# Optimization experiments

Measured on AMD Instinct MI355X. Metric: run time of the kernel, lower is better.

The kernel has to match this reference:

```python
import jax, jax.numpy as jnp
import numpy as np


def setup_inputs() -> dict:
    key = jax.random.key(0)
    k1, k2, k3 = jax.random.split(key, 3)
    B, T, D, H = 64, 512, 256, 512
    x = jax.random.normal(k1, (B, T, D), dtype=jnp.float32)
    W = jax.random.normal(k2, (D, 4 * H), dtype=jnp.float32) * 0.05
    U = jax.random.normal(k3, (H, 4 * H), dtype=jnp.float32) * 0.05
    b = jnp.zeros((4 * H,), dtype=jnp.float32)
    return {"x": x, "W": W, "U": U, "b": b, "batch": B}


def reference(x, W, U, b, batch):
    # Encoder(model_type='LSTM'): keras LSTMCell with recurrent_activation='tanh'
    # (so i/f/o gates use tanh, not sigmoid), activation='tanh'.
    B, T, D = x.shape
    H = U.shape[0]
    x_proj = jnp.einsum('btd,dk->btk', x, W) + b  # precompute input GEMM: [B,T,4H]

    def step(carry, xp_t):
        h, c = carry
        z = xp_t + h @ U                      # [B,4H]
        i, f, g, o = jnp.split(z, 4, axis=-1)  # keras gate order i,f,c,o
        i = jnp.tanh(i)
        f = jnp.tanh(f)
        g = jnp.tanh(g)
        o = jnp.tanh(o)
        c2 = f * c + i * g
        h2 = o * jnp.tanh(c2)
        return (h2, c2), h2

    h0 = jnp.zeros((B, H), dtype=x.dtype)
    c0 = jnp.zeros((B, H), dtype=x.dtype)
    (_, _), hs = jax.lax.scan(step, (h0, c0), x_proj.transpose(1, 0, 2))
    hs = hs.transpose(1, 0, 2)                              # [B,T,H]
    traj_h = jnp.concatenate([x, hs], axis=-1)              # [B,T,D+H]
    context_state = jnp.concatenate([x[:, -1, :], hs[:, -1, :]], axis=-1)  # [B,D+H]
    return context_state, traj_h
```

## Files before the change

### kernel.cpp

```cpp
#include <hip/hip_runtime.h>
#include <math.h>

#define BB 64
#define TT 512
#define DD 256
#define HH 512
#define GG 2048
#define KX 768
#define K4 192
#define CTXF 49152

__global__ void pack_vut(const float* __restrict__ Wm, const float* __restrict__ Um,
                         float* __restrict__ vut) {
    __shared__ float tile[32][33];
    int k0 = blockIdx.x * 32;
    int j0 = blockIdx.y * 32;
    int lx = threadIdx.x & 31;
    int ly = threadIdx.x >> 5;
    for (int r = ly; r < 32; r += 8) {
        int j = j0 + r, k = k0 + lx;
        tile[r][lx] = (j < DD) ? Wm[j * GG + k] : Um[(j - DD) * GG + k];
    }
    __syncthreads();
    for (int r = ly; r < 32; r += 8) {
        int k = k0 + r, j = j0 + lx;
        vut[(long)k * KX + j] = tile[lx][r];
    }
}

__global__ void init_state(float* __restrict__ h, unsigned* __restrict__ flags) {
    int idx = blockIdx.x * 256 + threadIdx.x;
    if (idx < 2 * BB * HH) h[idx] = 0.f;
    if (idx < 256) flags[idx] = 0u;
}

__global__ void xcopy(const float* __restrict__ x, float* __restrict__ out) {
    const long n_traj = (long)BB * TT * (DD / 4);
    long idx = (long)blockIdx.x * 256 + threadIdx.x;
    const float4* x4 = (const float4*)x;
    float4* out4 = (float4*)out;
    if (idx < n_traj) {
        long bt = idx / (DD / 4);
        int d4 = (int)(idx % (DD / 4));
        out4[(CTXF / 4) + bt * (KX / 4) + d4] = x4[idx];
    } else if (idx < n_traj + BB * (DD / 4)) {
        long f = idx - n_traj;
        int b = (int)(f / (DD / 4)), d4 = (int)(f % (DD / 4));
        out4[(long)b * (KX / 4) + d4] = x4[((long)b * TT + (TT - 1)) * (DD / 4) + d4];
    }
}

#define FMA4(A, Wv, Hv) \
    A.x += Wv.x * Hv.x; A.y += Wv.y * Hv.y; A.z += Wv.z * Hv.z; A.w += Wv.w * Hv.w;

__global__ __launch_bounds__(512) void lstm_persist(
    const float* __restrict__ vut, const float* __restrict__ bias,
    const float* __restrict__ x, float* __restrict__ h,
    unsigned* __restrict__ flags, float* __restrict__ out)
{
    __shared__ float4 w_lds[32 * K4];
    __shared__ float4 xh[16 * K4];
    __shared__ float  zsum[2][512];

    const int wg = blockIdx.x;
    const int jb = wg & 63;
    const int bg = wg >> 6;
    const int b0 = bg * 16;
    const int j0 = jb * 8;
    const int tid = threadIdx.x;
    const int ks = tid >> 5;
    const int ct = (tid >> 2) & 7;
    const int bt = tid & 3;

    const float4* x4g = (const float4*)x;
    float* lds_f = (float*)xh;

    for (int i = tid; i < 32 * K4; i += 512) {
        int r = i / K4;
        int k4 = i - r * K4;
        int col = (r >> 3) * HH + j0 + (r & 7);
        w_lds[r * K4 + (k4 ^ (r & 7))] =
            ((const float4*)(vut + (long)col * KX))[k4];
    }
    const int zr = tid >> 4;
    const float biasreg = bias[(zr >> 3) * HH + j0 + (zr & 7)];
    zsum[0][tid] = biasreg;

    float creg = 0.f;

    const int xb1 = tid >> 6, xk1 = tid & 63;
    const int xb2 = 8 + xb1;
    float4 xp1 = x4g[((long)(b0 + xb1) * TT + 0) * 64 + xk1];
    float4 xp2 = x4g[((long)(b0 + xb2) * TT + 0) * 64 + xk1];

    const float4* wl0 = &w_lds[(ct) * K4];
    const float4* wl1 = &w_lds[(8 + ct) * K4];
    const float4* wl2 = &w_lds[(16 + ct) * K4];
    const float4* wl3 = &w_lds[(24 + ct) * K4];
    const float4* xr0 = &xh[(bt) * K4];
    const float4* xr1 = &xh[(bt + 4) * K4];
    const float4* xr2 = &xh[(bt + 8) * K4];
    const float4* xr3 = &xh[(bt + 12) * K4];

    unsigned* const myflag = &flags[bg * 64 + jb];

    for (int t = 0; t < TT; ++t) {
        const int p = t & 1;
        const float* hp = h + p * (BB * HH);
        float* hn = h + (1 - p) * (BB * HH);

        xh[xb1 * K4 + (xk1 ^ (xb1 & 7))] = xp1;
        xh[xb2 * K4 + (xk1 ^ (xb2 & 7))] = xp2;
        if (t + 1 < TT) {
            xp1 = x4g[((long)(b0 + xb1) * TT + (t + 1)) * 64 + xk1];
            xp2 = x4g[((long)(b0 + xb2) * TT + (t + 1)) * 64 + xk1];
        }

        if (t > 0 && tid < 64) {
            const unsigned want = (unsigned)t;
            while (__hip_atomic_load(&flags[bg * 64 + tid], __ATOMIC_RELAXED,
                                     __HIP_MEMORY_SCOPE_AGENT) < want) {
                __builtin_amdgcn_s_sleep(2);
            }
        }
        __syncthreads();

        #pragma unroll
        for (int s = 0; s < 16; ++s) {
            int i = tid + s * 512;
            int b = i >> 9, j = i & 511;
            float v = __hip_atomic_load(&hp[(b0 + b) * HH + j], __ATOMIC_RELAXED,
                                        __HIP_MEMORY_SCOPE_AGENT);
            int k4 = 64 + (j >> 2);
            lds_f[(b * K4 + (k4 ^ (b & 7))) * 4 + (j & 3)] = v;
        }
        __syncthreads();

        float4 acc[4][4];
        #pragma unroll
        for (int g = 0; g < 4; ++g)
            #pragma unroll
            for (int s = 0; s < 4; ++s)
                acc[g][s] = make_float4(0.f, 0.f, 0.f, 0.f);

        #pragma unroll
        for (int it = 0; it < 12; ++it) {
            const int k4 = ks * 12 + it;
            const int kw  = k4 ^ ct;
            const int kh0 = k4 ^ bt;
            const int kh1 = k4 ^ (bt + 4);
            float4 w0v = wl0[kw], w1v = wl1[kw], w2v = wl2[kw], w3v = wl3[kw];
            float4 h0v = xr0[kh0], h1v = xr1[kh1], h2v = xr2[kh0], h3v = xr3[kh1];
            FMA4(acc[0][0], w0v, h0v); FMA4(acc[0][1], w0v, h1v);
            FMA4(acc[0][2], w0v, h2v); FMA4(acc[0][3], w0v, h3v);
            FMA4(acc[1][0], w1v, h0v); FMA4(acc[1][1], w1v, h1v);
            FMA4(acc[1][2], w1v, h2v); FMA4(acc[1][3], w1v, h3v);
            FMA4(acc[2][0], w2v, h0v); FMA4(acc[2][1], w2v, h1v);
            FMA4(acc[2][2], w2v, h2v); FMA4(acc[2][3], w2v, h3v);
            FMA4(acc[3][0], w3v, h0v); FMA4(acc[3][1], w3v, h1v);
            FMA4(acc[3][2], w3v, h2v); FMA4(acc[3][3], w3v, h3v);
        }
        #pragma unroll
        for (int g = 0; g < 4; ++g) {
            #pragma unroll
            for (int s = 0; s < 4; ++s) {
                float4 a = acc[g][s];
                float z = (a.x + a.y) + (a.z + a.w);
                atomicAdd(&zsum[p][(g * 8 + ct) * 16 + (bt + 4 * s)], z);
            }
        }
        __syncthreads();

        zsum[1 - p][tid] = biasreg;
        if (tid < 128) {
            const int b = tid >> 3, jj = tid & 7;
            float zi = zsum[p][(jj) * 16 + b];
            float zf = zsum[p][(8 + jj) * 16 + b];
            float zg = zsum[p][(16 + jj) * 16 + b];
            float zo = zsum[p][(24 + jj) * 16 + b];
            float iv = tanhf(zi);
            float fv = tanhf(zf);
            float gv = tanhf(zg);
            float ov = tanhf(zo);
            float c2 = fv * creg + iv * gv;
            float h2 = ov * tanhf(c2);
            creg = c2;
            __hip_atomic_store(&hn[(b0 + b) * HH + (j0 + jj)], h2,
                               __ATOMIC_RELAXED, __HIP_MEMORY_SCOPE_AGENT);
            out[CTXF + ((long)((b0 + b) * TT + t)) * KX + DD + (j0 + jj)] = h2;
            if (t == TT - 1) out[(long)(b0 + b) * KX + DD + (j0 + jj)] = h2;
        }
        __syncthreads();
        if (tid == 0) {
            __hip_atomic_store(myflag, (unsigned)(t + 1),
                               __ATOMIC_RELAXED, __HIP_MEMORY_SCOPE_AGENT);
        }
    }
}

extern "C" void kernel_launch(void* const* d_in, const int* in_sizes, int n_in,
                              void* d_out, int out_size, void* d_ws, size_t ws_size,
                              hipStream_t stream) {
    (void)in_sizes; (void)n_in; (void)out_size; (void)ws_size;
    const float* x    = (const float*)d_in[0];
    const float* Wm   = (const float*)d_in[1];
    const float* Um   = (const float*)d_in[2];
    const float* bias = (const float*)d_in[3];
    float* out = (float*)d_out;
    float* ws  = (float*)d_ws;

    float* vut      = ws;
    float* h        = ws + 1572864;
    unsigned* flags = (unsigned*)(ws + 1572864 + 65536);

    hipLaunchKernelGGL(pack_vut, dim3(64, 24), dim3(256), 0, stream, Wm, Um, vut);
    hipLaunchKernelGGL(init_state, dim3(256), dim3(256), 0, stream, h, flags);
    hipLaunchKernelGGL(xcopy, dim3(8209), dim3(256), 0, stream, x, out);

    void* args[] = {(void*)&vut, (void*)&bias, (void*)&x, (void*)&h,
                    (void*)&flags, (void*)&out};
    hipLaunchCooperativeKernel((const void*)lstm_persist, dim3(256), dim3(512),
                               args, 0, stream);
}
```

Baseline: 9.085 ms.

## Overlap x-part of recurrent GEMV with cross-block wait, widen h loads

```diff
diff --git a/kernel.cpp b/kernel.cpp
--- a/kernel.cpp
+++ b/kernel.cpp
@@ -73,7 +73,6 @@
     const int bt = tid & 3;
 
     const float4* x4g = (const float4*)x;
-    float* lds_f = (float*)xh;
 
     for (int i = tid; i < 32 * K4; i += 512) {
         int r = i / K4;
@@ -115,25 +114,6 @@
             xp1 = x4g[((long)(b0 + xb1) * TT + (t + 1)) * 64 + xk1];
             xp2 = x4g[((long)(b0 + xb2) * TT + (t + 1)) * 64 + xk1];
         }
-
-        if (t > 0 && tid < 64) {
-            const unsigned want = (unsigned)t;
-            while (__hip_atomic_load(&flags[bg * 64 + tid], __ATOMIC_RELAXED,
-                                     __HIP_MEMORY_SCOPE_AGENT) < want) {
-                __builtin_amdgcn_s_sleep(2);
-            }
-        }
-        __syncthreads();
-
-        #pragma unroll
-        for (int s = 0; s < 16; ++s) {
-            int i = tid + s * 512;
-            int b = i >> 9, j = i & 511;
-            float v = __hip_atomic_load(&hp[(b0 + b) * HH + j], __ATOMIC_RELAXED,
-                                        __HIP_MEMORY_SCOPE_AGENT);
-            int k4 = 64 + (j >> 2);
-            lds_f[(b * K4 + (k4 ^ (b & 7))) * 4 + (j & 3)] = v;
-        }
         __syncthreads();
 
         float4 acc[4][4];
@@ -144,8 +124,8 @@
                 acc[g][s] = make_float4(0.f, 0.f, 0.f, 0.f);
 
         #pragma unroll
-        for (int it = 0; it < 12; ++it) {
-            const int k4 = ks * 12 + it;
+        for (int it = 0; it < 4; ++it) {
+            const int k4 = ks * 4 + it;
             const int kw  = k4 ^ ct;
             const int kh0 = k4 ^ bt;
             const int kh1 = k4 ^ (bt + 4);
@@ -160,6 +140,53 @@
             FMA4(acc[3][0], w3v, h0v); FMA4(acc[3][1], w3v, h1v);
             FMA4(acc[3][2], w3v, h2v); FMA4(acc[3][3], w3v, h3v);
         }
+
+        if (t > 0 && tid < 64) {
+            const unsigned want = (unsigned)t;
+            while (__hip_atomic_load(&flags[bg * 64 + tid], __ATOMIC_RELAXED,
+                                     __HIP_MEMORY_SCOPE_AGENT) < want) {
+                __builtin_amdgcn_s_sleep(1);
+            }
+        }
+        __syncthreads();
+
+        const unsigned long long* hp64 = (const unsigned long long*)hp;
+        #pragma unroll
+        for (int s = 0; s < 4; ++s) {
+            int i = tid + s * 512;
+            int b = i >> 7, k4h = i & 127;
+            long base2 = (long)(b0 + b) * 256 + (long)k4h * 2;
+            unsigned long long lo = __hip_atomic_load(&hp64[base2], __ATOMIC_RELAXED,
+                                                      __HIP_MEMORY_SCOPE_AGENT);
+            unsigned long long hi = __hip_atomic_load(&hp64[base2 + 1], __ATOMIC_RELAXED,
+                                                      __HIP_MEMORY_SCOPE_AGENT);
+            float4 v;
+            v.x = __uint_as_float((unsigned)lo);
+            v.y = __uint_as_float((unsigned)(lo >> 32));
+            v.z = __uint_as_float((unsigned)hi);
+            v.w = __uint_as_float((unsigned)(hi >> 32));
+            int k4 = 64 + k4h;
+            xh[b * K4 + (k4 ^ (b & 7))] = v;
+        }
+        __syncthreads();
+
+        #pragma unroll
+        for (int it = 0; it < 8; ++it) {
+            const int k4 = 64 + ks * 8 + it;
+            const int kw  = k4 ^ ct;
+            const int kh0 = k4 ^ bt;
+            const int kh1 = k4 ^ (bt + 4);
+            float4 w0v = wl0[kw], w1v = wl1[kw], w2v = wl2[kw], w3v = wl3[kw];
+            float4 h0v = xr0[kh0], h1v = xr1[kh1], h2v = xr2[kh0], h3v = xr3[kh1];
+            FMA4(acc[0][0], w0v, h0v); FMA4(acc[0][1], w0v, h1v);
+            FMA4(acc[0][2], w0v, h2v); FMA4(acc[0][3], w0v, h3v);
+            FMA4(acc[1][0], w1v, h0v); FMA4(acc[1][1], w1v, h1v);
+            FMA4(acc[1][2], w1v, h2v); FMA4(acc[1][3], w1v, h3v);
+            FMA4(acc[2][0], w2v, h0v); FMA4(acc[2][1], w2v, h1v);
+            FMA4(acc[2][2], w2v, h2v); FMA4(acc[2][3], w2v, h3v);
+            FMA4(acc[3][0], w3v, h0v); FMA4(acc[3][1], w3v, h1v);
+            FMA4(acc[3][2], w3v, h2v); FMA4(acc[3][3], w3v, h3v);
+        }
         #pragma unroll
         for (int g = 0; g < 4; ++g) {
             #pragma unroll
@@ -172,6 +199,8 @@
         __syncthreads();
 
         zsum[1 - p][tid] = biasreg;
+        float h2 = 0.f;
+        int gb = 0, gj = 0;
         if (tid < 128) {
             const int b = tid >> 3, jj = tid & 7;
             float zi = zsum[p][(jj) * 16 + b];
@@ -183,17 +212,21 @@
             float gv = tanhf(zg);
             float ov = tanhf(zo);
             float c2 = fv * creg + iv * gv;
-            float h2 = ov * tanhf(c2);
+            h2 = ov * tanhf(c2);
             creg = c2;
-            __hip_atomic_store(&hn[(b0 + b) * HH + (j0 + jj)], h2,
+            gb = b0 + b; gj = j0 + jj;
+            __hip_atomic_store(&hn[gb * HH + gj], h2,
                                __ATOMIC_RELAXED, __HIP_MEMORY_SCOPE_AGENT);
-            out[CTXF + ((long)((b0 + b) * TT + t)) * KX + DD + (j0 + jj)] = h2;
-            if (t == TT - 1) out[(long)(b0 + b) * KX + DD + (j0 + jj)] = h2;
         }
         __syncthreads();
         if (tid == 0) {
             __hip_atomic_store(myflag, (unsigned)(t + 1),
                                __ATOMIC_RELAXED, __HIP_MEMORY_SCOPE_AGENT);
+        }
+
+        if (tid < 128) {
+            out[CTXF + ((long)(gb * TT + t)) * KX + DD + gj] = h2;
+            if (t == TT - 1) out[(long)gb * KX + DD + gj] = h2;
         }
     }
 }
```

After: 8.036 ms. -11.5%, faster.
